# Kernel tuning notes

Hardware: AMD Instinct MI355X
Metric: run time of the kernel (lower is better)

Reference implementation:

```python
import jax, jax.numpy as jnp
from jax import lax
import numpy as np

B, T, H, FUT = 2048, 1024, 128, 64

def setup_inputs() -> dict:
    key = jax.random.key(0)
    ks = jax.random.split(key, 7)
    s = 1.0 / np.sqrt(H)
    return {
        "x": jax.random.normal(ks[0], (B, T), dtype=jnp.float32),
        "W_ih": jax.random.uniform(ks[1], (H, 1), jnp.float32, -s, s),
        "W_hh": jax.random.uniform(ks[2], (H, H), jnp.float32, -s, s),
        "b_ih": jax.random.uniform(ks[3], (H,), jnp.float32, -s, s),
        "b_hh": jax.random.uniform(ks[4], (H,), jnp.float32, -s, s),
        "W_out": jax.random.uniform(ks[5], (1, H), jnp.float32, -s, s),
        "b_out": jax.random.uniform(ks[6], (1,), jnp.float32, -s, s),
        "future": FUT,
    }

def reference(x, W_ih, W_hh, b_ih, b_hh, W_out, b_out, future):
    n_samples = x.shape[0]
    n_hidden = W_hh.shape[0]
    h0 = jnp.zeros((n_samples, n_hidden), dtype=x.dtype)
    bias = b_ih + b_hh  # [H]

    def cell(h, inp):  # inp: [B] scalar input per sample
        # RNNCell: h' = tanh(x @ W_ih^T + b_ih + h @ W_hh^T + b_hh)
        h_new = jnp.tanh(inp[:, None] * W_ih[:, 0][None, :] + h @ W_hh.T + bias)
        out = h_new @ W_out.T + b_out  # [B, 1]
        return h_new, out[:, 0]

    # Teacher-forced steps over the input sequence
    h_last, outs = lax.scan(cell, h0, x.T)  # outs: [T, B]

    def fstep(carry, _):
        h, o = carry
        h_new, o_new = cell(h, o)
        return (h_new, o_new), o_new

    (_, _), fouts = lax.scan(fstep, (h_last, outs[-1]), None, length=future)  # [future, B]

    return jnp.concatenate([outs, fouts], axis=0).T  # [B, T+future]
```

## Files before the change

kernel.cpp:

```cpp
#include <hip/hip_runtime.h>
#include <stdint.h>
#include <math.h>


#define TLEN  1024
#define FUT   64
#define HID   128
#define SPB   4
#define NT    512
#define NSTEP (TLEN + FUT)

typedef float f32x4 __attribute__((ext_vector_type(4)));
typedef _Float16 f16x8 __attribute__((ext_vector_type(8)));
typedef uint32_t u32x4 __attribute__((ext_vector_type(4)));

__device__ __forceinline__ f16x8 asf16(u32x4 v) {
    return __builtin_bit_cast(f16x8, v);
}
__device__ __forceinline__ float fast_tanh(float v) {
    return 1.0f - 2.0f / (__expf(2.0f * v) + 1.0f);
}

__global__ __launch_bounds__(NT, 4) void rnn_kernel(
    const float* __restrict__ x,
    const float* __restrict__ W_ih,
    const float* __restrict__ W_hh,
    const float* __restrict__ b_ih,
    const float* __restrict__ b_hh,
    const float* __restrict__ W_out,
    const float* __restrict__ b_out,
    float* __restrict__ out)
{
    __shared__ __align__(16) unsigned short hbuf[2][SPB * HID];
    __shared__ __align__(16) float xstg[128][8];
    __shared__ __align__(16) float ring[2][SPB][68];

    const int tid  = threadIdx.x;
    const int lane = tid & 63;
    const int wid  = tid >> 6;
    const int l15  = lane & 15;
    const int g    = lane >> 4;
    const int s0   = blockIdx.x * SPB;

    const int j = 16 * wid + l15;
    f16x8 W0[4], Wo[4];
    {
        const float* r0 = W_hh + (size_t)j * HID;
        #pragma unroll
        for (int kt = 0; kt < 4; ++kt) {
            #pragma unroll
            for (int e = 0; e < 8; ++e) {
                const int k = 16 * e + 4 * kt + g;
                W0[kt][e] = (_Float16)r0[k];
                Wo[kt][e] = (l15 == 0) ? (_Float16)W_out[k] : (_Float16)0.0f;
            }
        }
    }
    const float bias0 = b_ih[j] + b_hh[j];
    const float wih0  = W_ih[j];
    const float bo    = b_out[0];

    const int s_ = l15 >> 2;
    int aoff[4];
    #pragma unroll
    for (int kt = 0; kt < 4; ++kt)
        aoff[kt] = s_ * 256 + (((4 * kt + g) * 16) ^ (s_ << 5));
    const int woff = g * 256 + ((l15 * 16 + 2 * wid) ^ (g << 5));

    for (int idx = tid; idx < SPB * HID; idx += NT)
        ((uint32_t*)hbuf)[idx] = 0;
    __syncthreads();

    u32x4 A_[4];
    #pragma unroll
    for (int kt = 0; kt < 4; ++kt) A_[kt] = (u32x4){0, 0, 0, 0};

    #pragma unroll 2
    for (int i = 0; i < TLEN; ++i) {
        const int p = i & 1;

        if ((i & 127) == 0) {
            const int t = tid & 127, s = tid >> 7;
            xstg[t][s] = x[(size_t)(s0 + s) * TLEN + (i + t)];
            __syncthreads();
        }
        if (i > 64 && (i & 63) == 1 && tid < 16 * SPB) {
            const int q = ((i - 65) >> 6) & 1;
            const int s = tid >> 4, c4 = (tid & 15) * 4;
            const f32x4 v = *(const f32x4*)&ring[q][s][c4];
            *(f32x4*)&out[(size_t)(s0 + s) * NSTEP + (i - 65) + c4] = v;
        }

        const char* hb = (const char*)hbuf[p];
        if ((l15 & 3) == 0) {
            #pragma unroll
            for (int kt = 0; kt < 4; ++kt)
                A_[kt] = *(const u32x4*)(hb + aoff[kt]);
        }

        f32x4 sA = {0.f,0.f,0.f,0.f}, ov = sA;
        #pragma unroll
        for (int kt = 0; kt < 4; ++kt) {
            sA = __builtin_amdgcn_mfma_f32_16x16x32_f16(asf16(A_[kt]), W0[kt], sA, 0, 0, 0);
            ov = __builtin_amdgcn_mfma_f32_16x16x32_f16(asf16(A_[kt]), Wo[kt], ov, 0, 0, 0);
        }

        if (i > 0 && wid == 0 && l15 == 0)
            ring[((i - 1) >> 6) & 1][g][(i - 1) & 63] = ov[0] + bo;

        const float in = xstg[i & 127][g];
        const float h0 = fast_tanh(sA[0] + bias0 + in * wih0);
        *(unsigned short*)((char*)hbuf[p ^ 1] + woff) =
            __builtin_bit_cast(unsigned short, (_Float16)h0);

        __syncthreads();
    }

    #pragma unroll 2
    for (int i = TLEN; i < NSTEP; ++i) {
        const int p = i & 1;

        if ((i & 63) == 1 && tid < 16 * SPB) {
            const int q = ((i - 65) >> 6) & 1;
            const int s = tid >> 4, c4 = (tid & 15) * 4;
            const f32x4 v = *(const f32x4*)&ring[q][s][c4];
            *(f32x4*)&out[(size_t)(s0 + s) * NSTEP + (i - 65) + c4] = v;
        }

        const char* hb = (const char*)hbuf[p];
        if ((l15 & 3) == 0) {
            #pragma unroll
            for (int kt = 0; kt < 4; ++kt)
                A_[kt] = *(const u32x4*)(hb + aoff[kt]);
        }

        f32x4 sA = {0.f,0.f,0.f,0.f}, ov = sA;
        #pragma unroll
        for (int kt = 0; kt < 4; ++kt) {
            sA = __builtin_amdgcn_mfma_f32_16x16x32_f16(asf16(A_[kt]), W0[kt], sA, 0, 0, 0);
            ov = __builtin_amdgcn_mfma_f32_16x16x32_f16(asf16(A_[kt]), Wo[kt], ov, 0, 0, 0);
        }
        const float oval = ov[0] + bo;
        if (wid == 0 && l15 == 0)
            ring[((i - 1) >> 6) & 1][g][(i - 1) & 63] = oval;

        const float in = __shfl(oval, g << 4);
        const float h0 = fast_tanh(sA[0] + bias0 + in * wih0);
        *(unsigned short*)((char*)hbuf[p ^ 1] + woff) =
            __builtin_bit_cast(unsigned short, (_Float16)h0);

        __syncthreads();
    }

    {
        const char* hb = (const char*)hbuf[NSTEP & 1];
        if ((l15 & 3) == 0) {
            #pragma unroll
            for (int kt = 0; kt < 4; ++kt)
                A_[kt] = *(const u32x4*)(hb + aoff[kt]);
        }
        f32x4 ov = {0.f,0.f,0.f,0.f};
        #pragma unroll
        for (int kt = 0; kt < 4; ++kt)
            ov = __builtin_amdgcn_mfma_f32_16x16x32_f16(asf16(A_[kt]), Wo[kt], ov, 0, 0, 0);
        if (wid == 0 && l15 == 0)
            ring[0][g][63] = ov[0] + bo;
    }
    __syncthreads();
    if (tid < 16 * SPB) {
        const int s = tid >> 4, c4 = (tid & 15) * 4;
        const f32x4 v = *(const f32x4*)&ring[0][s][c4];
        *(f32x4*)&out[(size_t)(s0 + s) * NSTEP + TLEN + c4] = v;
    }
}

extern "C" void kernel_launch(void* const* d_in, const int* in_sizes, int n_in,
                              void* d_out, int out_size, void* d_ws, size_t ws_size,
                              hipStream_t stream) {
    const float* x     = (const float*)d_in[0];
    const float* W_ih  = (const float*)d_in[1];
    const float* W_hh  = (const float*)d_in[2];
    const float* b_ih  = (const float*)d_in[3];
    const float* b_hh  = (const float*)d_in[4];
    const float* W_out = (const float*)d_in[5];
    const float* b_out = (const float*)d_in[6];
    float* out = (float*)d_out;

    dim3 grid(2048 / SPB);
    dim3 block(NT);
    rnn_kernel<<<grid, block, 0, stream>>>(x, W_ih, W_hh, b_ih, b_hh,
                                           W_out, b_out, out);
}
```

Before: 395.0 us.

## Shrink blocks to two samples and two waves, each wave computing four hidden tiles

Each block now handles 2 samples with 128 threads (2 waves) instead of 4 samples with 512 threads. Each wave issues four MFMA tiles per k-step, covering 64 hidden units, and writes packed fp16 pairs. The aim is a cheaper per-step __syncthreads across fewer waves and more independent blocks, which should help this latency-bound recurrence. In exchange, half of each MFMA's sample rows sit idle, register use per wave rises, and the grid doubles to 1024 blocks.

```diff
diff --git a/kernel.cpp b/kernel.cpp
--- a/kernel.cpp
+++ b/kernel.cpp
@@ -6,8 +6,8 @@
 #define TLEN  1024
 #define FUT   64
 #define HID   128
-#define SPB   4
-#define NT    512
+#define SPB   2
+#define NT    128
 #define NSTEP (TLEN + FUT)
 
 typedef float f32x4 __attribute__((ext_vector_type(4)));
@@ -20,8 +20,12 @@
 __device__ __forceinline__ float fast_tanh(float v) {
     return 1.0f - 2.0f / (__expf(2.0f * v) + 1.0f);
 }
-
-__global__ __launch_bounds__(NT, 4) void rnn_kernel(
+__device__ __forceinline__ uint32_t packh(float a, float b) {
+    return (uint32_t)__builtin_bit_cast(unsigned short, (_Float16)a)
+         | ((uint32_t)__builtin_bit_cast(unsigned short, (_Float16)b) << 16);
+}
+
+__global__ __launch_bounds__(NT, 2) void rnn_kernel(
     const float* __restrict__ x,
     const float* __restrict__ W_ih,
     const float* __restrict__ W_hh,
@@ -32,7 +36,7 @@
     float* __restrict__ out)
 {
     __shared__ __align__(16) unsigned short hbuf[2][SPB * HID];
-    __shared__ __align__(16) float xstg[128][8];
+    __shared__ __align__(16) float xstg[128][SPB];
     __shared__ __align__(16) float ring[2][SPB][68];
 
     const int tid  = threadIdx.x;
@@ -42,30 +46,38 @@
     const int g    = lane >> 4;
     const int s0   = blockIdx.x * SPB;
 
-    const int j = 16 * wid + l15;
-    f16x8 W0[4], Wo[4];
-    {
+    f16x8 W_[4][4], Wo[4];
+    float bias[4], wih[4];
+    #pragma unroll
+    for (int q = 0; q < 4; ++q) {
+        const int j = 64 * wid + 16 * q + l15;
         const float* r0 = W_hh + (size_t)j * HID;
         #pragma unroll
         for (int kt = 0; kt < 4; ++kt) {
             #pragma unroll
             for (int e = 0; e < 8; ++e) {
                 const int k = 16 * e + 4 * kt + g;
-                W0[kt][e] = (_Float16)r0[k];
-                Wo[kt][e] = (l15 == 0) ? (_Float16)W_out[k] : (_Float16)0.0f;
+                W_[q][kt][e] = (_Float16)r0[k];
             }
         }
-    }
-    const float bias0 = b_ih[j] + b_hh[j];
-    const float wih0  = W_ih[j];
-    const float bo    = b_out[0];
+        bias[q] = b_ih[j] + b_hh[j];
+        wih[q]  = W_ih[j];
+    }
+    #pragma unroll
+    for (int kt = 0; kt < 4; ++kt)
+        #pragma unroll
+        for (int e = 0; e < 8; ++e) {
+            const int k = 16 * e + 4 * kt + g;
+            Wo[kt][e] = (l15 == 0) ? (_Float16)W_out[k] : (_Float16)0.0f;
+        }
+    const float bo = b_out[0];
 
     const int s_ = l15 >> 2;
     int aoff[4];
     #pragma unroll
     for (int kt = 0; kt < 4; ++kt)
         aoff[kt] = s_ * 256 + (((4 * kt + g) * 16) ^ (s_ << 5));
-    const int woff = g * 256 + ((l15 * 16 + 2 * wid) ^ (g << 5));
+    const int woff = g * 256 + ((l15 * 16 + 8 * wid) ^ (g << 5));
 
     for (int idx = tid; idx < SPB * HID; idx += NT)
         ((uint32_t*)hbuf)[idx] = 0;
@@ -80,8 +92,12 @@
         const int p = i & 1;
 
         if ((i & 127) == 0) {
-            const int t = tid & 127, s = tid >> 7;
-            xstg[t][s] = x[(size_t)(s0 + s) * TLEN + (i + t)];
+            #pragma unroll
+            for (int pass = 0; pass < 2; ++pass) {
+                const int idx = pass * NT + tid;
+                const int t = idx & 127, s = idx >> 7;
+                xstg[t][s] = x[(size_t)(s0 + s) * TLEN + (i + t)];
+            }
             __syncthreads();
         }
         if (i > 64 && (i & 63) == 1 && tid < 16 * SPB) {
@@ -92,27 +108,35 @@
         }
 
         const char* hb = (const char*)hbuf[p];
-        if ((l15 & 3) == 0) {
+        if (l15 < 8 && (l15 & 3) == 0) {
             #pragma unroll
             for (int kt = 0; kt < 4; ++kt)
                 A_[kt] = *(const u32x4*)(hb + aoff[kt]);
         }
 
-        f32x4 sA = {0.f,0.f,0.f,0.f}, ov = sA;
+        f32x4 s0v = {0.f,0.f,0.f,0.f}, s1v = s0v, s2v = s0v, s3v = s0v, ov = s0v;
         #pragma unroll
         for (int kt = 0; kt < 4; ++kt) {
-            sA = __builtin_amdgcn_mfma_f32_16x16x32_f16(asf16(A_[kt]), W0[kt], sA, 0, 0, 0);
-            ov = __builtin_amdgcn_mfma_f32_16x16x32_f16(asf16(A_[kt]), Wo[kt], ov, 0, 0, 0);
-        }
-
-        if (i > 0 && wid == 0 && l15 == 0)
+            s0v = __builtin_amdgcn_mfma_f32_16x16x32_f16(asf16(A_[kt]), W_[0][kt], s0v, 0, 0, 0);
+            s1v = __builtin_amdgcn_mfma_f32_16x16x32_f16(asf16(A_[kt]), W_[1][kt], s1v, 0, 0, 0);
+            s2v = __builtin_amdgcn_mfma_f32_16x16x32_f16(asf16(A_[kt]), W_[2][kt], s2v, 0, 0, 0);
+            s3v = __builtin_amdgcn_mfma_f32_16x16x32_f16(asf16(A_[kt]), W_[3][kt], s3v, 0, 0, 0);
+            ov  = __builtin_amdgcn_mfma_f32_16x16x32_f16(asf16(A_[kt]), Wo[kt],    ov,  0, 0, 0);
+        }
+
+        if (i > 0 && wid == 0 && l15 == 0 && g < SPB)
             ring[((i - 1) >> 6) & 1][g][(i - 1) & 63] = ov[0] + bo;
 
-        const float in = xstg[i & 127][g];
-        const float h0 = fast_tanh(sA[0] + bias0 + in * wih0);
-        *(unsigned short*)((char*)hbuf[p ^ 1] + woff) =
-            __builtin_bit_cast(unsigned short, (_Float16)h0);
-
+        if (g < SPB) {
+            const float in = xstg[i & 127][g];
+            const float h0 = fast_tanh(s0v[0] + bias[0] + in * wih[0]);
+            const float h1 = fast_tanh(s1v[0] + bias[1] + in * wih[1]);
+            const float h2 = fast_tanh(s2v[0] + bias[2] + in * wih[2]);
+            const float h3 = fast_tanh(s3v[0] + bias[3] + in * wih[3]);
+            char* hw = (char*)hbuf[p ^ 1] + woff;
+            *(uint32_t*)(hw)     = packh(h0, h1);
+            *(uint32_t*)(hw + 4) = packh(h2, h3);
+        }
         __syncthreads();
     }
 
@@ -128,33 +152,41 @@
         }
 
         const char* hb = (const char*)hbuf[p];
-        if ((l15 & 3) == 0) {
+        if (l15 < 8 && (l15 & 3) == 0) {
             #pragma unroll
             for (int kt = 0; kt < 4; ++kt)
                 A_[kt] = *(const u32x4*)(hb + aoff[kt]);
         }
 
-        f32x4 sA = {0.f,0.f,0.f,0.f}, ov = sA;
+        f32x4 s0v = {0.f,0.f,0.f,0.f}, s1v = s0v, s2v = s0v, s3v = s0v, ov = s0v;
         #pragma unroll
         for (int kt = 0; kt < 4; ++kt) {
-            sA = __builtin_amdgcn_mfma_f32_16x16x32_f16(asf16(A_[kt]), W0[kt], sA, 0, 0, 0);
-            ov = __builtin_amdgcn_mfma_f32_16x16x32_f16(asf16(A_[kt]), Wo[kt], ov, 0, 0, 0);
+            s0v = __builtin_amdgcn_mfma_f32_16x16x32_f16(asf16(A_[kt]), W_[0][kt], s0v, 0, 0, 0);
+            s1v = __builtin_amdgcn_mfma_f32_16x16x32_f16(asf16(A_[kt]), W_[1][kt], s1v, 0, 0, 0);
+            s2v = __builtin_amdgcn_mfma_f32_16x16x32_f16(asf16(A_[kt]), W_[2][kt], s2v, 0, 0, 0);
+            s3v = __builtin_amdgcn_mfma_f32_16x16x32_f16(asf16(A_[kt]), W_[3][kt], s3v, 0, 0, 0);
+            ov  = __builtin_amdgcn_mfma_f32_16x16x32_f16(asf16(A_[kt]), Wo[kt],    ov,  0, 0, 0);
         }
         const float oval = ov[0] + bo;
-        if (wid == 0 && l15 == 0)
+        if (wid == 0 && l15 == 0 && g < SPB)
             ring[((i - 1) >> 6) & 1][g][(i - 1) & 63] = oval;
 
-        const float in = __shfl(oval, g << 4);
-        const float h0 = fast_tanh(sA[0] + bias0 + in * wih0);
-        *(unsigned short*)((char*)hbuf[p ^ 1] + woff) =
-            __builtin_bit_cast(unsigned short, (_Float16)h0);
-
+        const float in = __shfl(oval, (g & 1) << 4);
+        if (g < SPB) {
+            const float h0 = fast_tanh(s0v[0] + bias[0] + in * wih[0]);
+            const float h1 = fast_tanh(s1v[0] + bias[1] + in * wih[1]);
+            const float h2 = fast_tanh(s2v[0] + bias[2] + in * wih[2]);
+            const float h3 = fast_tanh(s3v[0] + bias[3] + in * wih[3]);
+            char* hw = (char*)hbuf[p ^ 1] + woff;
+            *(uint32_t*)(hw)     = packh(h0, h1);
+            *(uint32_t*)(hw + 4) = packh(h2, h3);
+        }
         __syncthreads();
     }
 
     {
         const char* hb = (const char*)hbuf[NSTEP & 1];
-        if ((l15 & 3) == 0) {
+        if (l15 < 8 && (l15 & 3) == 0) {
             #pragma unroll
             for (int kt = 0; kt < 4; ++kt)
                 A_[kt] = *(const u32x4*)(hb + aoff[kt]);
@@ -163,7 +195,7 @@
         #pragma unroll
         for (int kt = 0; kt < 4; ++kt)
             ov = __builtin_amdgcn_mfma_f32_16x16x32_f16(asf16(A_[kt]), Wo[kt], ov, 0, 0, 0);
-        if (wid == 0 && l15 == 0)
+        if (wid == 0 && l15 == 0 && g < SPB)
             ring[0][g][63] = ov[0] + bo;
     }
     __syncthreads();
```

Result: slower. 736.9 us (+86.6%).
